# Performance work log

Measured on AMD Instinct MI355X. Metric: run time of the kernel, lower is better.

## Reference

```python
import jax, jax.numpy as jnp
import numpy as np

H = 64      # hidden_num
IN = 8      # input_num
P = 8192    # number of POIs
N = 8192    # graph nodes
SCALING = 2.0
NEG_INF = -9e15
ALPHA = 0.2  # leaky relu slope in GAT


def gru_cell(x, h, Wih, Whh, bih, bhh):
    # torch.nn.GRUCell math
    gi = x @ Wih.T + bih
    gh = h @ Whh.T + bhh
    ir, iz, inn = jnp.split(gi, 3, axis=1)
    hr, hz, hn = jnp.split(gh, 3, axis=1)
    r = jax.nn.sigmoid(ir + hr)
    z = jax.nn.sigmoid(iz + hz)
    n = jnp.tanh(inn + r * hn)
    return (1.0 - z) * n + z * h


def gat_layer(h, adj, W, a):
    # pyGAT GraphAttentionLayer (eval mode, no dropout)
    Wh = h @ W                      # [N, F']
    F = W.shape[1]
    e1 = Wh @ a[:F]                 # [N, 1]
    e2 = Wh @ a[F:]                 # [N, 1]
    e = jax.nn.leaky_relu(e1 + e2.T, negative_slope=ALPHA)  # [N, N]
    e = jnp.where(adj > 0, e, NEG_INF)
    attn = jax.nn.softmax(e, axis=1)
    return attn @ Wh                # [N, F']


def gat_forward(nodes, adj, gatW, gatA, gatWout, gatAout):
    # 4 heads, concat, then output layer; log_softmax at the end
    heads = [jax.nn.elu(gat_layer(nodes, adj, gatW[k], gatA[k])) for k in range(gatW.shape[0])]
    x1 = jnp.concatenate(heads, axis=1)                      # [N, 16]
    out = jax.nn.elu(gat_layer(x1, adj, gatWout, gatAout))   # [N, 2]
    return jax.nn.log_softmax(out, axis=1)


def setup_inputs() -> dict:
    key = jax.random.key(0)
    ks = jax.random.split(key, 24)
    s = 0.1  # keep params small so exp() terms stay in range
    inp = {
        "x": jax.random.normal(ks[0], (1, IN), jnp.float32),
        "user": jax.random.uniform(ks[1], (1, 1), jnp.float32),
        "nextHid": jax.random.normal(ks[2], (1, H), jnp.float32),
        "periodHid": jax.random.normal(ks[3], (1, H), jnp.float32),
        "qhh": jnp.ones((H, H), jnp.float32),
        "aH": jnp.zeros((H, H), jnp.float32),
        "poi_loc": jax.random.normal(ks[4], (P, 2), jnp.float32),
        "poi_dist": jax.random.uniform(ks[5], (P,), jnp.float32),
        "nodes": jax.random.normal(ks[6], (N, 4), jnp.float32),
        "pre": 0,
    }
    # sparse-ish random adjacency (avg degree ~32) with self loops, dense [N,N] as in pyGAT
    mask = (jax.random.uniform(ks[7], (N, N)) < (32.0 / N)).astype(jnp.float32)
    inp["edges"] = jnp.maximum(mask, jnp.eye(N, dtype=jnp.float32))
    # learned parameters
    inp["w"] = jax.random.normal(ks[8], (1, 1), jnp.float32) * s
    inp["Wih1"] = jax.random.normal(ks[9], (3 * H, IN), jnp.float32) * s
    inp["Whh1"] = jax.random.normal(ks[10], (3 * H, H), jnp.float32) * s
    inp["bih1"] = jax.random.normal(ks[11], (3 * H,), jnp.float32) * s
    inp["bhh1"] = jax.random.normal(ks[12], (3 * H,), jnp.float32) * s
    inp["Wih3"] = jax.random.normal(ks[13], (3 * H, IN + 1), jnp.float32) * s
    inp["Whh3"] = jax.random.normal(ks[14], (3 * H, H), jnp.float32) * s
    inp["bih3"] = jax.random.normal(ks[15], (3 * H,), jnp.float32) * s
    inp["bhh3"] = jax.random.normal(ks[16], (3 * H,), jnp.float32) * s
    inp["gatW"] = jax.random.normal(ks[17], (4, 4, 4), jnp.float32) * s
    inp["gatA"] = jax.random.normal(ks[18], (4, 8, 1), jnp.float32) * s
    inp["gatWout"] = jax.random.normal(ks[19], (16, 2), jnp.float32) * s
    inp["gatAout"] = jax.random.normal(ks[20], (4, 1), jnp.float32) * s
    return inp


def reference(x, user, nextHid, periodHid, qhh, aH, poi_loc, poi_dist, nodes, edges, pre,
              w, Wih1, Whh1, bih1, bhh1, Wih3, Whh3, bih3, bhh3,
              gatW, gatA, gatWout, gatAout):
    # --- sequence GRU step (lastTime is None branch -> GRUCell1) ---
    nextHid = gru_cell(x, nextHid, Wih1, Whh1, bih1, bhh1)          # [1, H]
    h = nextHid[0]                                                   # [H]

    # --- distance-weighted POI attention, fully vectorized ---
    d = jnp.exp(-poi_dist / SCALING)                                 # [P]
    # qLis_p = (nextHid^T) @ w @ eLi_p  -> outer(h, loc_p) * w
    E = jnp.exp(w[0, 0] * h[None, :, None] * poi_loc[:, None, :] * d[:, None, None])  # [P, H, 2]
    allwe = E.sum(axis=0)                                            # [H, 2]
    cL = jnp.einsum('phe,pe->h', E / allwe, poi_loc)[:, None]        # [H, 1]

    # --- periodicity GRU + attention ---
    xin = jnp.concatenate([user, x], axis=1)                         # [1, IN+1]
    periodHid = gru_cell(xin, periodHid, Wih3, Whh3, bih3, bhh3)     # [1, H]
    qhi = jnp.exp(nextHid.T @ periodHid)                             # [H, H]
    qhh = qhh + qhi
    aH = aH + qhi / qhh
    cP = aH @ periodHid.T                                            # [H, 1]

    # --- GAT over the POI graph ---
    outGAT = gat_forward(nodes, edges, gatW, gatA, gatWout, gatAout) # [N, 2]

    # --- scoring: anw_p = max_j (g_p . loc_p) * mL_j ---
    mL = jnp.concatenate([nextHid, cL.T, cP.T], axis=1)              # [1, 3H]
    g = jax.lax.dynamic_slice_in_dim(outGAT, pre, P, axis=0)         # [P, 2]
    s = jnp.einsum('pk,pk->p', g, poi_loc)                           # [P]
    anw_logits = jnp.max(s[:, None] * mL, axis=1)                    # [P]
    anw = jax.nn.softmax(anw_logits)
    value, index = jax.lax.top_k(anw, 5)
    return (nextHid, periodHid, qhh, aH, index)
```

## Files before the change

### kernel.cpp

```cpp
#include <hip/hip_runtime.h>
#include <math.h>

#define H64 64
#define IN8 8
#define PNUM 8192
#define NNUM 8192
#define ALPHA_LR 0.2f
#define MAXDEG 128
#define SEGCAP 96
#define FRONTB 81

typedef float f32x4 __attribute__((ext_vector_type(4)));

constexpr int WS_NH = 0;
constexpr int WS_PH = 64;
constexpr int WS_CP = 128;
constexpr int WS_MAXML = 256;
constexpr int WS_MINML = 257;
constexpr int WS_PART = 320;
constexpr int WS_NF2 = 262656;
constexpr int WS_LOGITS = 295424;
constexpr int WS_DEG = 303616;
constexpr int WS_NBR = 311808;
constexpr int WS_TPART = 574016;
constexpr int WS_TCNT = 574400;

__device__ __forceinline__ float sigm_(float x) { return 1.0f / (1.0f + expf(-x)); }
__device__ __forceinline__ float elu_(float x) { return x > 0.0f ? x : expm1f(x); }

__global__ __launch_bounds__(256) void k_main(
    const float* __restrict__ x, const float* __restrict__ user,
    const float* __restrict__ nh0, const float* __restrict__ ph0,
    const float* __restrict__ qhh_in, const float* __restrict__ aH_in,
    const float* __restrict__ loc, const float* __restrict__ dist,
    const float* __restrict__ wscal,
    const float* __restrict__ Wih1, const float* __restrict__ Whh1,
    const float* __restrict__ bih1, const float* __restrict__ bhh1,
    const float* __restrict__ Wih3, const float* __restrict__ Whh3,
    const float* __restrict__ bih3, const float* __restrict__ bhh3,
    const float* __restrict__ nodes, const float* __restrict__ gatW,
    const float* __restrict__ gatA, const float* __restrict__ Wout,
    const float* __restrict__ Aout, const float* __restrict__ edges,
    float* __restrict__ ws, float* __restrict__ out,
    int* __restrict__ deg, int* __restrict__ nbr) {
    __shared__ float snh[64], sph[64];
    __shared__ float sl[256], sde[128];
    __shared__ int s_seg[4][SEGCAP];
    __shared__ int s_cnt[4];
    __shared__ int s_all[4 * SEGCAP];
    __shared__ float s_head[4][5];
    const int b = blockIdx.x, tid = threadIdx.x;

    if (b < FRONTB) {
        if (tid < 64) {
            int t = tid;
            float gir = bih1[t], giz = bih1[H64 + t], gin = bih1[2 * H64 + t];
            for (int c = 0; c < IN8; ++c) {
                float xv = x[c];
                gir += xv * Wih1[t * IN8 + c];
                giz += xv * Wih1[(H64 + t) * IN8 + c];
                gin += xv * Wih1[(2 * H64 + t) * IN8 + c];
            }
            float ghr = bhh1[t], ghz = bhh1[H64 + t], ghn = bhh1[2 * H64 + t];
            for (int c = 0; c < H64; ++c) {
                float hv = nh0[c];
                ghr += hv * Whh1[t * H64 + c];
                ghz += hv * Whh1[(H64 + t) * H64 + c];
                ghn += hv * Whh1[(2 * H64 + t) * H64 + c];
            }
            float r = sigm_(gir + ghr), z = sigm_(giz + ghz);
            float n = tanhf(gin + r * ghn);
            snh[t] = (1.0f - z) * n + z * nh0[t];
        } else if (tid < 128) {
            int t = tid - 64;
            const int INC = IN8 + 1;
            float gir = bih3[t], giz = bih3[H64 + t], gin = bih3[2 * H64 + t];
            for (int c = 0; c < INC; ++c) {
                float xv = (c == 0) ? user[0] : x[c - 1];
                gir += xv * Wih3[t * INC + c];
                giz += xv * Wih3[(H64 + t) * INC + c];
                gin += xv * Wih3[(2 * H64 + t) * INC + c];
            }
            float ghr = bhh3[t], ghz = bhh3[H64 + t], ghn = bhh3[2 * H64 + t];
            for (int c = 0; c < H64; ++c) {
                float hv = ph0[c];
                ghr += hv * Whh3[t * H64 + c];
                ghz += hv * Whh3[(H64 + t) * H64 + c];
                ghn += hv * Whh3[(2 * H64 + t) * H64 + c];
            }
            float r = sigm_(gir + ghr), z = sigm_(giz + ghz);
            float n = tanhf(gin + r * ghn);
            sph[t] = (1.0f - z) * n + z * ph0[t];
        }
        __syncthreads();

        if (b < 16) {
            int w = tid >> 6, j = tid & 63;
            int i = b * 4 + w;
            float qhi = expf(snh[i] * sph[j]);
            float qn = qhh_in[i * H64 + j] + qhi;
            float an = aH_in[i * H64 + j] + qhi / qn;
            out[128 + i * H64 + j] = qn;
            out[128 + H64 * H64 + i * H64 + j] = an;
            float v = an * sph[j];
            for (int off = 32; off >= 1; off >>= 1) v += __shfl_xor(v, off);
            if (j == 0) ws[WS_CP + i] = v;
        } else if (b < 80) {
            int p0 = (b - 16) * 128;
            sl[tid] = loc[p0 * 2 + tid];
            if (tid < 128) sde[tid] = expf(-dist[p0 + tid] * 0.5f);
            __syncthreads();
            int h = tid & 63, sub = tid >> 6;
            float a = wscal[0] * snh[h];
            float4 s = make_float4(0.f, 0.f, 0.f, 0.f);
            for (int pp = sub * 32; pp < sub * 32 + 32; ++pp) {
                float l0 = sl[2 * pp], l1 = sl[2 * pp + 1], dd = sde[pp];
                float E0 = expf(a * l0 * dd);
                float E1 = expf(a * l1 * dd);
                s.x += E0; s.y += E0 * l0; s.z += E1; s.w += E1 * l1;
            }
            ((float4*)(ws + WS_PART))[((b - 16) * 4 + sub) * 64 + h] = s;
        } else {
            if (tid < 64) { ws[WS_NH + tid] = snh[tid]; out[tid] = snh[tid]; }
            else if (tid < 128) { int t = tid - 64; ws[WS_PH + t] = sph[t]; out[64 + t] = sph[t]; }
        }
        return;
    }

    const int wave = tid >> 6, lane = tid & 63;
    const int row = b - FRONTB;
    const f32x4* erow = (const f32x4*)(edges + (size_t)row * NNUM);
    const unsigned long long lmask = (1ull << lane) - 1ull;

    float wk[4][4], a1v[4], a2v[4];
#pragma unroll
    for (int r = 0; r < 4; ++r)
#pragma unroll
        for (int f = 0; f < 4; ++f) wk[r][f] = gatW[wave * 16 + r * 4 + f];
#pragma unroll
    for (int f = 0; f < 4; ++f) { a1v[f] = gatA[wave * 8 + f]; a2v[f] = gatA[wave * 8 + 4 + f]; }

    float4 ndr = *(const float4*)(nodes + (size_t)row * 4);
    float e1k;
    {
        float w0 = ndr.x * wk[0][0] + ndr.y * wk[1][0] + ndr.z * wk[2][0] + ndr.w * wk[3][0];
        float w1 = ndr.x * wk[0][1] + ndr.y * wk[1][1] + ndr.z * wk[2][1] + ndr.w * wk[3][1];
        float w2 = ndr.x * wk[0][2] + ndr.y * wk[1][2] + ndr.z * wk[2][2] + ndr.w * wk[3][2];
        float w3 = ndr.x * wk[0][3] + ndr.y * wk[1][3] + ndr.z * wk[2][3] + ndr.w * wk[3][3];
        e1k = w0 * a1v[0] + w1 * a1v[1] + w2 * a1v[2] + w3 * a1v[3];
    }

    f32x4 bchunk[8];
#pragma unroll
    for (int u = 0; u < 8; ++u)
        bchunk[u] = __builtin_nontemporal_load(&erow[wave * 512 + u * 64 + lane]);
    int base = 0;
#pragma unroll
    for (int u = 0; u < 8; ++u) {
        f32x4 cv = bchunk[u];
        float mx01 = fmaxf(cv[0], cv[1]);
        float mx23 = fmaxf(cv[2], cv[3]);
        bool any = fmaxf(mx01, mx23) > 0.0f;
        unsigned long long am = __ballot(any);
        if (am == 0ull) continue;
        int jb = wave * 2048 + u * 256 + lane * 4;
#pragma unroll
        for (int c = 0; c < 4; ++c) {
            bool hit = cv[c] > 0.0f;
            unsigned long long mask = __ballot(hit);
            if (hit) {
                int pos = base + __popcll(mask & lmask);
                if (pos < SEGCAP) s_seg[wave][pos] = jb + c;
            }
            base += __popcll(mask);
        }
    }
    if (lane == 0) s_cnt[wave] = base < SEGCAP ? base : SEGCAP;
    __syncthreads();

    int c0 = s_cnt[0], c1 = s_cnt[1], c2 = s_cnt[2], c3 = s_cnt[3];
    int offw = (wave > 0 ? c0 : 0) + (wave > 1 ? c1 : 0) + (wave > 2 ? c2 : 0);
    int cw = s_cnt[wave];
    for (int s = lane; s < cw; s += 64) s_all[offw + s] = s_seg[wave][s];
    __syncthreads();

    int d = c0 + c1 + c2 + c3;
    int dcl = d < MAXDEG ? d : MAXDEG;
    if (tid == 0) deg[row] = dcl;
    for (int s = tid; s < dcl; s += 256) nbr[row * MAXDEG + s] = s_all[s];

    float den = 0.0f, a0 = 0.0f, a1 = 0.0f, a2 = 0.0f, a3 = 0.0f;
    for (int s = lane; s < d; s += 64) {
        int j = s_all[s];
        float4 nd = *(const float4*)(nodes + (size_t)j * 4);
        float w0 = nd.x * wk[0][0] + nd.y * wk[1][0] + nd.z * wk[2][0] + nd.w * wk[3][0];
        float w1 = nd.x * wk[0][1] + nd.y * wk[1][1] + nd.z * wk[2][1] + nd.w * wk[3][1];
        float w2 = nd.x * wk[0][2] + nd.y * wk[1][2] + nd.z * wk[2][2] + nd.w * wk[3][2];
        float w3 = nd.x * wk[0][3] + nd.y * wk[1][3] + nd.z * wk[2][3] + nd.w * wk[3][3];
        float e2 = w0 * a2v[0] + w1 * a2v[1] + w2 * a2v[2] + w3 * a2v[3];
        float e = e1k + e2;
        float lr = e >= 0.0f ? e : ALPHA_LR * e;
        float p = __expf(lr);
        den += p;
        a0 += p * w0; a1 += p * w1; a2 += p * w2; a3 += p * w3;
    }
    for (int off = 1; off < 64; off <<= 1) {
        den += __shfl_xor(den, off);
        a0 += __shfl_xor(a0, off);
        a1 += __shfl_xor(a1, off);
        a2 += __shfl_xor(a2, off);
        a3 += __shfl_xor(a3, off);
    }
    if (lane == 0) {
        s_head[wave][0] = den;
        s_head[wave][1] = a0; s_head[wave][2] = a1;
        s_head[wave][3] = a2; s_head[wave][4] = a3;
    }
    __syncthreads();
    if (tid == 0) {
        float x1v[16];
#pragma unroll
        for (int k = 0; k < 4; ++k) {
            float dk = s_head[k][0];
#pragma unroll
            for (int f = 0; f < 4; ++f) x1v[k * 4 + f] = elu_(s_head[k][1 + f] / dk);
        }
        float v0 = 0, v1 = 0;
#pragma unroll
        for (int c = 0; c < 16; ++c) {
            v0 += x1v[c] * Wout[c * 2 + 0];
            v1 += x1v[c] * Wout[c * 2 + 1];
        }
        float ee1 = v0 * Aout[0] + v1 * Aout[1];
        float ee2 = v0 * Aout[2] + v1 * Aout[3];
        float4* nf2 = (float4*)(ws + WS_NF2 + row * 4);
        *nf2 = make_float4(ee1, ee2, v0, v1);
    }
}

__global__ __launch_bounds__(256) void k_mid(const float* __restrict__ loc,
                                             const int* __restrict__ pre_p,
                                             float* __restrict__ ws,
                                             const int* __restrict__ deg,
                                             const int* __restrict__ nbr) {
    __shared__ float red[4][64][4];
    const int tid = threadIdx.x;

    if (blockIdx.x == 2048) {
        if (tid == 0) *((int*)(ws + WS_TCNT)) = 0;
        int h = tid & 63, g = tid >> 6;
        const float4* part = (const float4*)(ws + WS_PART);
        float4 s = make_float4(0.f, 0.f, 0.f, 0.f);
        for (int seg = g; seg < 256; seg += 4) {
            float4 p = part[seg * 64 + h];
            s.x += p.x; s.y += p.y; s.z += p.z; s.w += p.w;
        }
        red[g][h][0] = s.x; red[g][h][1] = s.y; red[g][h][2] = s.z; red[g][h][3] = s.w;
        __syncthreads();
        if (tid < 64) {
            float sd0 = 0, sn0 = 0, sd1 = 0, sn1 = 0;
            for (int g2 = 0; g2 < 4; ++g2) {
                sd0 += red[g2][tid][0]; sn0 += red[g2][tid][1];
                sd1 += red[g2][tid][2]; sn1 += red[g2][tid][3];
            }
            float cl = sn0 / sd0 + sn1 / sd1;
            float av = ws[WS_NH + tid], cv = ws[WS_CP + tid];
            float mx = fmaxf(fmaxf(av, cl), cv);
            float mn = fminf(fminf(av, cl), cv);
            for (int off = 32; off >= 1; off >>= 1) {
                mx = fmaxf(mx, __shfl_xor(mx, off));
                mn = fminf(mn, __shfl_xor(mn, off));
            }
            if (tid == 0) { ws[WS_MAXML] = mx; ws[WS_MINML] = mn; }
        }
        return;
    }

    const int wave = tid >> 6, lane = tid & 63;
    const int row = blockIdx.x * 4 + wave;
    const float4* nf2 = (const float4*)(ws + WS_NF2);
    float e1r = ws[WS_NF2 + row * 4];
    int d = deg[row];
    const int* nrow = nbr + row * MAXDEG;
    float den = 0, a0 = 0, a1 = 0;
    for (int s = lane; s < d; s += 64) {
        int j = nrow[s];
        float4 nf = nf2[j];
        float e = e1r + nf.y;
        float lr = e >= 0.0f ? e : ALPHA_LR * e;
        float p = __expf(lr);
        den += p; a0 += p * nf.z; a1 += p * nf.w;
    }
    for (int off = 1; off < 64; off <<= 1) {
        den += __shfl_xor(den, off);
        a0 += __shfl_xor(a0, off);
        a1 += __shfl_xor(a1, off);
    }
    if (lane == 0) {
        float o0 = elu_(a0 / den), o1 = elu_(a1 / den);
        float mm = fmaxf(o0, o1);
        float lse = mm + logf(expf(o0 - mm) + expf(o1 - mm));
        float l0 = o0 - lse, l1 = o1 - lse;
        int start = pre_p[0];
        if (start < 0) start = 0;
        if (start > NNUM - PNUM) start = NNUM - PNUM;
        int p = row - start;
        if (p >= 0 && p < PNUM)
            ws[WS_LOGITS + p] = l0 * loc[p * 2 + 0] + l1 * loc[p * 2 + 1];
    }
}

__global__ __launch_bounds__(256) void k_top5(float* __restrict__ ws, float* __restrict__ out) {
    __shared__ unsigned long long sk[256 * 5];
    __shared__ int slast;
    const int b = blockIdx.x, t = threadIdx.x;
    float mx = ws[WS_MAXML], mn = ws[WS_MINML];
    int p = b * 256 + t;
    float s = ws[WS_LOGITS + p];
    float val = s > 0.0f ? s * mx : s * mn;
    unsigned u = __float_as_uint(val);
    u = (u & 0x80000000u) ? ~u : (u | 0x80000000u);
    unsigned long long key = ((unsigned long long)u << 32) | (unsigned)(PNUM - 1 - p);
    sk[t * 5] = key;
#pragma unroll
    for (int q = 1; q < 5; ++q) sk[t * 5 + q] = 0ull;
    __syncthreads();
    for (int stride = 128; stride >= 1; stride >>= 1) {
        if (t < stride) {
            unsigned long long r[5];
            int ia = 0, ib = 0;
            int ab = t * 5, bb = (t + stride) * 5;
#pragma unroll
            for (int q = 0; q < 5; ++q) {
                unsigned long long av = sk[ab + ia], bv = sk[bb + ib];
                if (av >= bv) { r[q] = av; ++ia; } else { r[q] = bv; ++ib; }
            }
#pragma unroll
            for (int q = 0; q < 5; ++q) sk[ab + q] = r[q];
        }
        __syncthreads();
    }
    unsigned long long* part = (unsigned long long*)(ws + WS_TPART);
    int* cnt = (int*)(ws + WS_TCNT);
    if (t < 5)
        __hip_atomic_store(&part[b * 5 + t], sk[t], __ATOMIC_RELAXED, __HIP_MEMORY_SCOPE_AGENT);
    if (t == 0) {
        asm volatile("s_waitcnt vmcnt(0)" ::: "memory");
        int old = __hip_atomic_fetch_add(cnt, 1, __ATOMIC_RELAXED, __HIP_MEMORY_SCOPE_AGENT);
        slast = (old == 31) ? 1 : 0;
    }
    __syncthreads();
    if (!slast) return;
    unsigned long long k2 = (t < 160)
        ? __hip_atomic_load(&part[t], __ATOMIC_RELAXED, __HIP_MEMORY_SCOPE_AGENT) : 0ull;
    __syncthreads();
    sk[t * 5] = k2;
#pragma unroll
    for (int q = 1; q < 5; ++q) sk[t * 5 + q] = 0ull;
    __syncthreads();
    for (int stride = 128; stride >= 1; stride >>= 1) {
        if (t < stride) {
            unsigned long long r[5];
            int ia = 0, ib = 0;
            int ab = t * 5, bb = (t + stride) * 5;
#pragma unroll
            for (int q = 0; q < 5; ++q) {
                unsigned long long av = sk[ab + ia], bv = sk[bb + ib];
                if (av >= bv) { r[q] = av; ++ia; } else { r[q] = bv; ++ib; }
            }
#pragma unroll
            for (int q = 0; q < 5; ++q) sk[ab + q] = r[q];
        }
        __syncthreads();
    }
    if (t == 0) {
#pragma unroll
        for (int q = 0; q < 5; ++q)
            out[8320 + q] = (float)(PNUM - 1 - (int)(sk[q] & 0xFFFFFFFFull));
    }
}

extern "C" void kernel_launch(void* const* d_in, const int* in_sizes, int n_in,
                              void* d_out, int out_size, void* d_ws, size_t ws_size,
                              hipStream_t stream) {
    const float* x        = (const float*)d_in[0];
    const float* user     = (const float*)d_in[1];
    const float* nextHid  = (const float*)d_in[2];
    const float* periodHid= (const float*)d_in[3];
    const float* qhh      = (const float*)d_in[4];
    const float* aH       = (const float*)d_in[5];
    const float* poi_loc  = (const float*)d_in[6];
    const float* poi_dist = (const float*)d_in[7];
    const float* nodes    = (const float*)d_in[8];
    const int*   pre      = (const int*)d_in[9];
    const float* edges    = (const float*)d_in[10];
    const float* w        = (const float*)d_in[11];
    const float* Wih1     = (const float*)d_in[12];
    const float* Whh1     = (const float*)d_in[13];
    const float* bih1     = (const float*)d_in[14];
    const float* bhh1     = (const float*)d_in[15];
    const float* Wih3     = (const float*)d_in[16];
    const float* Whh3     = (const float*)d_in[17];
    const float* bih3     = (const float*)d_in[18];
    const float* bhh3     = (const float*)d_in[19];
    const float* gatW     = (const float*)d_in[20];
    const float* gatA     = (const float*)d_in[21];
    const float* gatWout  = (const float*)d_in[22];
    const float* gatAout  = (const float*)d_in[23];
    float* out = (float*)d_out;
    float* ws  = (float*)d_ws;
    int* deg = (int*)(ws + WS_DEG);
    int* nbr = (int*)(ws + WS_NBR);

    hipLaunchKernelGGL(k_main, dim3(FRONTB + NNUM), dim3(256), 0, stream,
                       x, user, nextHid, periodHid, qhh, aH, poi_loc, poi_dist, w,
                       Wih1, Whh1, bih1, bhh1, Wih3, Whh3, bih3, bhh3,
                       nodes, gatW, gatA, gatWout, gatAout, edges, ws, out, deg, nbr);
    hipLaunchKernelGGL(k_mid, dim3(2049), dim3(256), 0, stream, poi_loc, pre, ws, deg, nbr);
    hipLaunchKernelGGL(k_top5, dim3(32), dim3(256), 0, stream, ws, out);
}
```

Measured before the change: 75.67 us.

## Fuse GAT output layer and top-5 kernels into one launch with spin-wait barrier

```diff
diff --git a/kernel.cpp b/kernel.cpp
--- a/kernel.cpp
+++ b/kernel.cpp
@@ -9,6 +9,10 @@
 #define MAXDEG 128
 #define SEGCAP 96
 #define FRONTB 81
+#define TB_GAT 1024
+#define TB_CL  1024
+#define TB_RED 1025
+#define TB_N   1057
 
 typedef float f32x4 __attribute__((ext_vector_type(4)));
 
@@ -23,7 +27,8 @@
 constexpr int WS_DEG = 303616;
 constexpr int WS_NBR = 311808;
 constexpr int WS_TPART = 574016;
-constexpr int WS_TCNT = 574400;
+constexpr int WS_CNTA = 574400;
+constexpr int WS_CNTB = 574401;
 
 __device__ __forceinline__ float sigm_(float x) { return 1.0f / (1.0f + expf(-x)); }
 __device__ __forceinline__ float elu_(float x) { return x > 0.0f ? x : expm1f(x); }
@@ -121,6 +126,7 @@
             }
             ((float4*)(ws + WS_PART))[((b - 16) * 4 + sub) * 64 + h] = s;
         } else {
+            if (tid == 0) { ((int*)(ws + WS_CNTA))[0] = 0; ((int*)(ws + WS_CNTB))[0] = 0; }
             if (tid < 64) { ws[WS_NH + tid] = snh[tid]; out[tid] = snh[tid]; }
             else if (tid < 128) { int t = tid - 64; ws[WS_PH + t] = sph[t]; out[64 + t] = sph[t]; }
         }
@@ -238,21 +244,71 @@
     }
 }
 
-__global__ __launch_bounds__(256) void k_mid(const float* __restrict__ loc,
-                                             const int* __restrict__ pre_p,
-                                             float* __restrict__ ws,
-                                             const int* __restrict__ deg,
-                                             const int* __restrict__ nbr) {
+__global__ __launch_bounds__(256) void k_tail(const float* __restrict__ loc,
+                                              const int* __restrict__ pre_p,
+                                              float* __restrict__ ws,
+                                              const int* __restrict__ deg,
+                                              const int* __restrict__ nbr,
+                                              float* __restrict__ out) {
     __shared__ float red[4][64][4];
-    const int tid = threadIdx.x;
-
-    if (blockIdx.x == 2048) {
-        if (tid == 0) *((int*)(ws + WS_TCNT)) = 0;
+    __shared__ unsigned long long sk[256 * 5];
+    __shared__ int slast;
+    const int b = blockIdx.x, tid = threadIdx.x;
+    const int wave = tid >> 6, lane = tid & 63;
+    float* logits = ws + WS_LOGITS;
+    int* cntA = (int*)(ws + WS_CNTA);
+    int* cntB = (int*)(ws + WS_CNTB);
+    unsigned long long* part = (unsigned long long*)(ws + WS_TPART);
+
+    if (b < TB_GAT) {
+        int start = pre_p[0];
+        if (start < 0) start = 0;
+        if (start > NNUM - PNUM) start = NNUM - PNUM;
+        const float4* nf2 = (const float4*)(ws + WS_NF2);
+#pragma unroll
+        for (int rr = 0; rr < 2; ++rr) {
+            int row = b * 8 + wave * 2 + rr;
+            float e1r = ws[WS_NF2 + row * 4];
+            int d = deg[row];
+            const int* nrow = nbr + row * MAXDEG;
+            float den = 0, a0 = 0, a1 = 0;
+            for (int s = lane; s < d; s += 64) {
+                int j = nrow[s];
+                float4 nf = nf2[j];
+                float e = e1r + nf.y;
+                float lr = e >= 0.0f ? e : ALPHA_LR * e;
+                float p = __expf(lr);
+                den += p; a0 += p * nf.z; a1 += p * nf.w;
+            }
+            for (int off = 1; off < 64; off <<= 1) {
+                den += __shfl_xor(den, off);
+                a0 += __shfl_xor(a0, off);
+                a1 += __shfl_xor(a1, off);
+            }
+            if (lane == 0) {
+                float o0 = elu_(a0 / den), o1 = elu_(a1 / den);
+                float mm = fmaxf(o0, o1);
+                float lse = mm + logf(expf(o0 - mm) + expf(o1 - mm));
+                float l0 = o0 - lse, l1 = o1 - lse;
+                int p = row - start;
+                if (p >= 0 && p < PNUM) {
+                    float sval = l0 * loc[p * 2 + 0] + l1 * loc[p * 2 + 1];
+                    __hip_atomic_store(&logits[p], sval, __ATOMIC_RELAXED, __HIP_MEMORY_SCOPE_AGENT);
+                }
+            }
+        }
+        asm volatile("s_waitcnt vmcnt(0)" ::: "memory");
+        __syncthreads();
+        if (tid == 0) __hip_atomic_fetch_add(cntA, 1, __ATOMIC_RELAXED, __HIP_MEMORY_SCOPE_AGENT);
+        return;
+    }
+
+    if (b == TB_CL) {
         int h = tid & 63, g = tid >> 6;
-        const float4* part = (const float4*)(ws + WS_PART);
+        const float4* partc = (const float4*)(ws + WS_PART);
         float4 s = make_float4(0.f, 0.f, 0.f, 0.f);
         for (int seg = g; seg < 256; seg += 4) {
-            float4 p = part[seg * 64 + h];
+            float4 p = partc[seg * 64 + h];
             s.x += p.x; s.y += p.y; s.z += p.z; s.w += p.w;
         }
         red[g][h][0] = s.x; red[g][h][1] = s.y; red[g][h][2] = s.z; red[g][h][3] = s.w;
@@ -271,65 +327,40 @@
                 mx = fmaxf(mx, __shfl_xor(mx, off));
                 mn = fminf(mn, __shfl_xor(mn, off));
             }
-            if (tid == 0) { ws[WS_MAXML] = mx; ws[WS_MINML] = mn; }
-        }
+            if (tid == 0) {
+                __hip_atomic_store(&ws[WS_MAXML], mx, __ATOMIC_RELAXED, __HIP_MEMORY_SCOPE_AGENT);
+                __hip_atomic_store(&ws[WS_MINML], mn, __ATOMIC_RELAXED, __HIP_MEMORY_SCOPE_AGENT);
+            }
+        }
+        asm volatile("s_waitcnt vmcnt(0)" ::: "memory");
+        __syncthreads();
+        if (tid == 0) __hip_atomic_fetch_add(cntA, 1, __ATOMIC_RELAXED, __HIP_MEMORY_SCOPE_AGENT);
         return;
     }
 
-    const int wave = tid >> 6, lane = tid & 63;
-    const int row = blockIdx.x * 4 + wave;
-    const float4* nf2 = (const float4*)(ws + WS_NF2);
-    float e1r = ws[WS_NF2 + row * 4];
-    int d = deg[row];
-    const int* nrow = nbr + row * MAXDEG;
-    float den = 0, a0 = 0, a1 = 0;
-    for (int s = lane; s < d; s += 64) {
-        int j = nrow[s];
-        float4 nf = nf2[j];
-        float e = e1r + nf.y;
-        float lr = e >= 0.0f ? e : ALPHA_LR * e;
-        float p = __expf(lr);
-        den += p; a0 += p * nf.z; a1 += p * nf.w;
-    }
-    for (int off = 1; off < 64; off <<= 1) {
-        den += __shfl_xor(den, off);
-        a0 += __shfl_xor(a0, off);
-        a1 += __shfl_xor(a1, off);
-    }
-    if (lane == 0) {
-        float o0 = elu_(a0 / den), o1 = elu_(a1 / den);
-        float mm = fmaxf(o0, o1);
-        float lse = mm + logf(expf(o0 - mm) + expf(o1 - mm));
-        float l0 = o0 - lse, l1 = o1 - lse;
-        int start = pre_p[0];
-        if (start < 0) start = 0;
-        if (start > NNUM - PNUM) start = NNUM - PNUM;
-        int p = row - start;
-        if (p >= 0 && p < PNUM)
-            ws[WS_LOGITS + p] = l0 * loc[p * 2 + 0] + l1 * loc[p * 2 + 1];
-    }
-}
-
-__global__ __launch_bounds__(256) void k_top5(float* __restrict__ ws, float* __restrict__ out) {
-    __shared__ unsigned long long sk[256 * 5];
-    __shared__ int slast;
-    const int b = blockIdx.x, t = threadIdx.x;
-    float mx = ws[WS_MAXML], mn = ws[WS_MINML];
-    int p = b * 256 + t;
-    float s = ws[WS_LOGITS + p];
+    const int rid = b - TB_RED;
+    if (tid == 0) {
+        while (__hip_atomic_load(cntA, __ATOMIC_RELAXED, __HIP_MEMORY_SCOPE_AGENT) < TB_GAT + 1)
+            __builtin_amdgcn_s_sleep(2);
+    }
+    __syncthreads();
+    float mx = __hip_atomic_load(&ws[WS_MAXML], __ATOMIC_RELAXED, __HIP_MEMORY_SCOPE_AGENT);
+    float mn = __hip_atomic_load(&ws[WS_MINML], __ATOMIC_RELAXED, __HIP_MEMORY_SCOPE_AGENT);
+    int p = rid * 256 + tid;
+    float s = __hip_atomic_load(&logits[p], __ATOMIC_RELAXED, __HIP_MEMORY_SCOPE_AGENT);
     float val = s > 0.0f ? s * mx : s * mn;
     unsigned u = __float_as_uint(val);
     u = (u & 0x80000000u) ? ~u : (u | 0x80000000u);
     unsigned long long key = ((unsigned long long)u << 32) | (unsigned)(PNUM - 1 - p);
-    sk[t * 5] = key;
-#pragma unroll
-    for (int q = 1; q < 5; ++q) sk[t * 5 + q] = 0ull;
+    sk[tid * 5] = key;
+#pragma unroll
+    for (int q = 1; q < 5; ++q) sk[tid * 5 + q] = 0ull;
     __syncthreads();
     for (int stride = 128; stride >= 1; stride >>= 1) {
-        if (t < stride) {
+        if (tid < stride) {
             unsigned long long r[5];
             int ia = 0, ib = 0;
-            int ab = t * 5, bb = (t + stride) * 5;
+            int ab = tid * 5, bb = (tid + stride) * 5;
 #pragma unroll
             for (int q = 0; q < 5; ++q) {
                 unsigned long long av = sk[ab + ia], bv = sk[bb + ib];
@@ -340,29 +371,27 @@
         }
         __syncthreads();
     }
-    unsigned long long* part = (unsigned long long*)(ws + WS_TPART);
-    int* cnt = (int*)(ws + WS_TCNT);
-    if (t < 5)
-        __hip_atomic_store(&part[b * 5 + t], sk[t], __ATOMIC_RELAXED, __HIP_MEMORY_SCOPE_AGENT);
-    if (t == 0) {
+    if (tid < 5)
+        __hip_atomic_store(&part[rid * 5 + tid], sk[tid], __ATOMIC_RELAXED, __HIP_MEMORY_SCOPE_AGENT);
+    if (tid == 0) {
         asm volatile("s_waitcnt vmcnt(0)" ::: "memory");
-        int old = __hip_atomic_fetch_add(cnt, 1, __ATOMIC_RELAXED, __HIP_MEMORY_SCOPE_AGENT);
+        int old = __hip_atomic_fetch_add(cntB, 1, __ATOMIC_RELAXED, __HIP_MEMORY_SCOPE_AGENT);
         slast = (old == 31) ? 1 : 0;
     }
     __syncthreads();
     if (!slast) return;
-    unsigned long long k2 = (t < 160)
-        ? __hip_atomic_load(&part[t], __ATOMIC_RELAXED, __HIP_MEMORY_SCOPE_AGENT) : 0ull;
-    __syncthreads();
-    sk[t * 5] = k2;
-#pragma unroll
-    for (int q = 1; q < 5; ++q) sk[t * 5 + q] = 0ull;
+    unsigned long long k2 = (tid < 160)
+        ? __hip_atomic_load(&part[tid], __ATOMIC_RELAXED, __HIP_MEMORY_SCOPE_AGENT) : 0ull;
+    __syncthreads();
+    sk[tid * 5] = k2;
+#pragma unroll
+    for (int q = 1; q < 5; ++q) sk[tid * 5 + q] = 0ull;
     __syncthreads();
     for (int stride = 128; stride >= 1; stride >>= 1) {
-        if (t < stride) {
+        if (tid < stride) {
             unsigned long long r[5];
             int ia = 0, ib = 0;
-            int ab = t * 5, bb = (t + stride) * 5;
+            int ab = tid * 5, bb = (tid + stride) * 5;
 #pragma unroll
             for (int q = 0; q < 5; ++q) {
                 unsigned long long av = sk[ab + ia], bv = sk[bb + ib];
@@ -373,7 +402,7 @@
         }
         __syncthreads();
     }
-    if (t == 0) {
+    if (tid == 0) {
 #pragma unroll
         for (int q = 0; q < 5; ++q)
             out[8320 + q] = (float)(PNUM - 1 - (int)(sk[q] & 0xFFFFFFFFull));
@@ -416,6 +445,5 @@
                        x, user, nextHid, periodHid, qhh, aH, poi_loc, poi_dist, w,
                        Wih1, Whh1, bih1, bhh1, Wih3, Whh3, bih3, bhh3,
                        nodes, gatW, gatA, gatWout, gatAout, edges, ws, out, deg, nbr);
-    hipLaunchKernelGGL(k_mid, dim3(2049), dim3(256), 0, stream, poi_loc, pre, ws, deg, nbr);
-    hipLaunchKernelGGL(k_top5, dim3(32), dim3(256), 0, stream, ws, out);
+    hipLaunchKernelGGL(k_tail, dim3(TB_N), dim3(256), 0, stream, poi_loc, pre, ws, deg, nbr, out);
 }
```

Measured after the change: 86.90 us. 1.15x slower.
